# Optimization experiments

Hardware: AMD Instinct MI355X
Metric: run time of the kernel (lower is better)

Reference implementation:

```python
import jax, jax.numpy as jnp
import numpy as np

IN_DIM = 128
MEM_DIM = 256
NUM_CLASSES = 12
NUM_LEVELS = 17  # complete binary tree, N = 2**17 - 1 = 131071 nodes


def setup_inputs() -> dict:
    key = jax.random.key(0)
    ks = jax.random.split(key, 7)
    N = 2 ** NUM_LEVELS - 1
    s = 1.0 / np.sqrt(MEM_DIM)  # PyTorch LSTMCell/Linear init scale
    return {
        "x": jax.random.normal(ks[0], (N, IN_DIM), dtype=jnp.float32),
        "W_ih": jax.random.uniform(ks[1], (4 * MEM_DIM, IN_DIM), jnp.float32, -s, s),
        "b_ih": jax.random.uniform(ks[2], (4 * MEM_DIM,), jnp.float32, -s, s),
        "W_hh": jax.random.uniform(ks[3], (4 * MEM_DIM, MEM_DIM), jnp.float32, -s, s),
        "b_hh": jax.random.uniform(ks[4], (4 * MEM_DIM,), jnp.float32, -s, s),
        "W_fc": jax.random.uniform(ks[5], (NUM_CLASSES, MEM_DIM), jnp.float32, -s, s),
        "b_fc": jax.random.uniform(ks[6], (NUM_CLASSES,), jnp.float32, -s, s),
        "num_levels": NUM_LEVELS,
    }


def reference(x, W_ih, b_ih, W_hh, b_hh, W_fc, b_fc, num_levels):
    # Complete binary tree in BFS order: level l occupies nodes [2^l-1, 2^(l+1)-2];
    # children of level-l nodes are exactly the (contiguous) level-(l+1) nodes.
    mem = W_hh.shape[1]
    h_below = None
    c_below = None
    for l in reversed(range(num_levels)):
        n = 2 ** l
        x_l = x[n - 1:2 * n - 1]  # [n, in_dim] nodes at this level
        if h_below is None:  # leaves: zero child state
            ch_h = jnp.zeros((n, mem), dtype=x.dtype)
            ch_c = ch_h
        else:  # sum the two children's (h, c), as the recursion accumulates
            ch_h = h_below.reshape(n, 2, mem).sum(axis=1)
            ch_c = c_below.reshape(n, 2, mem).sum(axis=1)
        # PyTorch LSTMCell: gates = x W_ih^T + b_ih + h W_hh^T + b_hh, chunks i,f,g,o
        gates = x_l @ W_ih.T + b_ih + ch_h @ W_hh.T + b_hh  # [n, 4*mem]
        i, f, g, o = jnp.split(gates, 4, axis=-1)
        c_new = jax.nn.sigmoid(f) * ch_c + jax.nn.sigmoid(i) * jnp.tanh(g)
        h_new = jax.nn.sigmoid(o) * jnp.tanh(c_new)
        h_below, c_below = h_new, c_new
    # Original applies FC to state[1] == cell state c of the root (kept faithfully).
    return c_below[:1] @ W_fc.T + b_fc  # [1, num_classes]
```

## Files before the change

kernel.cpp:

```cpp
#include <hip/hip_runtime.h>
#include <hip/hip_bf16.h>
#include <cstddef>

#define IN_DIM 128
#define MEM 256
#define KTOT 384
#define NLEAF 65536
#define NBLK_TAIL 8

typedef float f32x4 __attribute__((ext_vector_type(4)));
typedef short s16x8 __attribute__((ext_vector_type(8)));
typedef unsigned int u32;

__device__ inline unsigned short f2bf(float f){
    unsigned int u = __builtin_bit_cast(unsigned int, f);
    u += 0x7fff + ((u >> 16) & 1);
    return (unsigned short)(u >> 16);
}

__device__ inline void gld_lds16(const void* g, void* l){
    __builtin_amdgcn_global_load_lds((const __attribute__((address_space(1))) u32*)g,
                                     (__attribute__((address_space(3))) u32*)l, 16, 0, 0);
}

__device__ inline float fsigm(float x){
    return __builtin_amdgcn_rcpf(1.f + __expf(-x));
}
__device__ inline float ftanh(float x){
    return 2.f * __builtin_amdgcn_rcpf(1.f + __expf(-2.f * x)) - 1.f;
}

__host__ __device__ inline size_t offA(int l){
    if (l == 16) return 0;
    return 8388608u + 384u * (65536u - (1u << (l + 1)));
}
#define ARENA_ELEMS 33554048u
#define ARENA_PAD   65536u

__device__ inline void grid_barrier(unsigned* ctr, unsigned target){
    __syncthreads();
    if (threadIdx.x == 0){
        __threadfence();
        __hip_atomic_fetch_add(ctr, 1u, __ATOMIC_RELEASE, __HIP_MEMORY_SCOPE_AGENT);
        while (__hip_atomic_load(ctr, __ATOMIC_RELAXED, __HIP_MEMORY_SCOPE_AGENT) < target)
            __builtin_amdgcn_s_sleep(2);
    }
    __syncthreads();
    __threadfence();
}

__global__ void pack_kernel(const float* __restrict__ x,
                            const float* __restrict__ W_ih, const float* __restrict__ b_ih,
                            const float* __restrict__ W_hh, const float* __restrict__ b_hh,
                            unsigned short* __restrict__ Wp, float* __restrict__ bp,
                            unsigned short* __restrict__ Aarena, unsigned* __restrict__ ctr){
    const int stride = gridDim.x * blockDim.x;
    const int tid0 = blockIdx.x * blockDim.x + threadIdx.x;
    if (tid0 == 0){ ctr[0] = 0; }

    for (int g = tid0; g < 1024 * 48; g += stride){
        int row = g / 48, ko = (g - row * 48) * 8;
        const float* s = (ko < IN_DIM) ? (W_ih + (size_t)row * IN_DIM + ko)
                                       : (W_hh + (size_t)row * MEM + (ko - IN_DIM));
        f32x4 v0 = *(const f32x4*)s, v1 = *(const f32x4*)(s + 4);
        s16x8 o;
        #pragma unroll
        for (int e = 0; e < 4; ++e){ o[e] = (short)f2bf(v0[e]); o[4+e] = (short)f2bf(v1[e]); }
        *(s16x8*)(Wp + (size_t)row * KTOT + ko) = o;
        if (ko == 0) bp[row] = b_ih[row] + b_hh[row];
    }

    const int TOTAL_G = 131071 * 16;
    for (int g = tid0; g < TOTAL_G; g += stride){
        int i  = g >> 4;
        int ko = (g & 15) * 8;
        int l  = 31 - __clz(i + 1);
        int j  = i + 1 - (1 << l);
        size_t dst = offA(l) + (size_t)j * ((l == 16) ? 128 : 384) + ko;
        const f32x4* s = (const f32x4*)(x + (size_t)i * IN_DIM + ko);
        f32x4 v0 = s[0], v1 = s[1];
        s16x8 o;
        #pragma unroll
        for (int e = 0; e < 4; ++e){ o[e] = (short)f2bf(v0[e]); o[4+e] = (short)f2bf(v1[e]); }
        *(s16x8*)(Aarena + dst) = o;
    }
}

#define BM 128
#define KC 64

template<int NK>
__global__ __launch_bounds__(256) void gemm_lstm_kernel(
    const unsigned short* __restrict__ A, int n,
    const unsigned short* __restrict__ Wp, const float* __restrict__ bp,
    const float* __restrict__ csum_in, int leaf,
    unsigned short* __restrict__ A_next, float* __restrict__ csum_out)
{
    __shared__ __align__(16) unsigned short As[2][BM * KC];
    __shared__ __align__(16) unsigned short Bs[2][BM * KC];

    const int tid  = threadIdx.x;
    const int lane = tid & 63;
    const int wid  = tid >> 6;
    const int wm   = wid >> 1;
    const int wc   = wid & 1;
    const int row0 = blockIdx.x * BM;
    const int m0   = blockIdx.y * 32;

    const int srow = lane >> 3;
    const int scol = ((lane & 7) ^ srow) * 8;

    const int mg = m0 + wc * 16 + (lane & 15);

    const float b0 = bp[0 * 256 + mg];
    const float b1 = bp[1 * 256 + mg];
    const float b2 = bp[2 * 256 + mg];
    const float b3 = bp[3 * 256 + mg];
    float cpre[4][4];
    if (!leaf){
        #pragma unroll
        for (int r = 0; r < 4; ++r){
            const int base = row0 + wm * 64 + r * 16 + (lane >> 4) * 4;
            #pragma unroll
            for (int e = 0; e < 4; ++e)
                cpre[r][e] = csum_in[(size_t)(base + e) * MEM + mg];
        }
    } else {
        #pragma unroll
        for (int r = 0; r < 4; ++r)
            #pragma unroll
            for (int e = 0; e < 4; ++e) cpre[r][e] = 0.f;
    }

    f32x4 acc[4][4];
    #pragma unroll
    for (int r = 0; r < 4; ++r)
        #pragma unroll
        for (int q = 0; q < 4; ++q)
            acc[r][q] = (f32x4){0.f, 0.f, 0.f, 0.f};

    auto stage = [&](int d, int kk){
        char* asb = (char*)As[d];
        char* bsb = (char*)Bs[d];
        #pragma unroll
        for (int q = 0; q < 4; ++q){
            int t = wid * 4 + q;
            int r = t * 8 + srow;
            gld_lds16(A + (size_t)(row0 + r) * NK + kk + scol, asb + t * 1024);
        }
        #pragma unroll
        for (int q = 0; q < 4; ++q){
            int t = wid * 4 + q;
            int b = t * 8 + srow;
            int grow = (b >> 5) * 256 + m0 + (b & 31);
            gld_lds16(Wp + (size_t)grow * KTOT + kk + scol, bsb + t * 1024);
        }
    };

    constexpr int nIter = NK / KC;
    stage(0, 0);
    int buf = 0;
    #pragma unroll
    for (int it = 0; it < nIter; ++it){
        if (it + 1 < nIter){
            stage(buf ^ 1, (it + 1) * KC);
            asm volatile("s_waitcnt vmcnt(8)" ::: "memory");
        } else {
            asm volatile("s_waitcnt vmcnt(0)" ::: "memory");
        }
        __builtin_amdgcn_s_barrier();
        const unsigned short* Ab = As[buf];
        const unsigned short* Bb = Bs[buf];
        #pragma unroll
        for (int ks = 0; ks < 2; ++ks){
            const int slot = ks * 4 + (lane >> 4);
            const int kb = (slot ^ (lane & 7)) * 8;
            s16x8 a[4], b[4];
            #pragma unroll
            for (int r = 0; r < 4; ++r)
                a[r] = *(const s16x8*)(Ab + (wm * 64 + r * 16 + (lane & 15)) * KC + kb);
            #pragma unroll
            for (int q = 0; q < 4; ++q)
                b[q] = *(const s16x8*)(Bb + (q * 32 + wc * 16 + (lane & 15)) * KC + kb);
            #pragma unroll
            for (int r = 0; r < 4; ++r)
                #pragma unroll
                for (int q = 0; q < 4; ++q)
                    acc[r][q] = __builtin_amdgcn_mfma_f32_16x16x32_bf16(a[r], b[q], acc[r][q], 0, 0, 0);
        }
        __builtin_amdgcn_s_barrier();
        buf ^= 1;
    }

    #pragma unroll
    for (int r = 0; r < 4; ++r){
        const int base = row0 + wm * 64 + r * 16 + (lane >> 4) * 4;
        float cn[4], hn[4];
        #pragma unroll
        for (int e = 0; e < 4; ++e){
            float iv = acc[r][0][e] + b0;
            float fv = acc[r][1][e] + b1;
            float gv = acc[r][2][e] + b2;
            float ov = acc[r][3][e] + b3;
            float c  = fsigm(fv) * cpre[r][e] + fsigm(iv) * ftanh(gv);
            cn[e] = c;
            hn[e] = fsigm(ov) * ftanh(c);
        }
        if (base < n){
            int p0 = base >> 1;
            A_next[(size_t)p0 * KTOT + IN_DIM + mg] = f2bf(hn[0] + hn[1]);
            csum_out[(size_t)p0 * MEM + mg] = cn[0] + cn[1];
        }
        if (base + 2 < n){
            int p1 = (base >> 1) + 1;
            A_next[(size_t)p1 * KTOT + IN_DIM + mg] = f2bf(hn[2] + hn[3]);
            csum_out[(size_t)p1 * MEM + mg] = cn[2] + cn[3];
        }
    }
}

__global__ __launch_bounds__(256) void tail_kernel(
    const unsigned short* __restrict__ arena,
    const unsigned short* __restrict__ Wp, const float* __restrict__ bp,
    float* cs_in, float* cs_out,
    float* __restrict__ c_root,
    const float* __restrict__ W_fc, const float* __restrict__ b_fc,
    float* __restrict__ out, unsigned* __restrict__ ctr)
{
    __shared__ __align__(16) unsigned short WpL[128 * KTOT];
    __shared__ __align__(16) unsigned short AL[64 * KTOT];

    const int tid  = threadIdx.x;
    const int lane = tid & 63;
    const int wid  = tid >> 6;
    const int wm   = wid >> 1;
    const int wc   = wid & 1;
    const int m0   = blockIdx.x * 32;
    const int mg   = m0 + wc * 16 + (lane & 15);

    #pragma unroll
    for (int i = 0; i < 24; ++i){
        int p0 = wid * 1536 + i * 64;
        int p  = p0 + lane;
        int lrow  = p / 48;
        int pslot = p % 48;
        int lslot = pslot ^ (lrow & 7);
        int grow  = (lrow >> 5) * 256 + m0 + (lrow & 31);
        gld_lds16(Wp + (size_t)grow * KTOT + lslot * 8, (char*)WpL + (size_t)p0 * 16);
    }

    const float b0 = bp[0 * 256 + mg];
    const float b1 = bp[1 * 256 + mg];
    const float b2 = bp[2 * 256 + mg];
    const float b3 = bp[3 * 256 + mg];

    asm volatile("s_waitcnt vmcnt(0)" ::: "memory");
    __builtin_amdgcn_s_barrier();

    unsigned gen = 0;
    for (int l = 7; l >= 0; --l){
        const int n = 1 << l;
        const unsigned short* Al = arena + offA(l);
        const int nhalf = (n > 64) ? (n >> 6) : 1;

        for (int h = 0; h < nhalf; ++h){
            const int r0 = h * 64;
            const int rows = (n < 64) ? n : 64;

            const int nslots = rows * 48;
            for (int t = 0; t * 256 < nslots; ++t){
                int pbase = t * 256 + wid * 64;
                int p = pbase + lane;
                if (p < nslots){
                    int row   = p / 48;
                    int pslot = p - row * 48;
                    int lslot = pslot ^ (row & 7);
                    gld_lds16(Al + (size_t)(r0 + row) * KTOT + lslot * 8,
                              (char*)AL + (size_t)pbase * 16);
                }
            }

            float cpre[2][4];
            #pragma unroll
            for (int r = 0; r < 2; ++r){
                const int base = r0 + wm * 32 + r * 16 + (lane >> 4) * 4;
                #pragma unroll
                for (int e = 0; e < 4; ++e)
                    cpre[r][e] = cs_in[(size_t)(base + e) * MEM + mg];
            }

            asm volatile("s_waitcnt vmcnt(0)" ::: "memory");
            __builtin_amdgcn_s_barrier();

            f32x4 acc[2][4];
            #pragma unroll
            for (int r = 0; r < 2; ++r)
                #pragma unroll
                for (int q = 0; q < 4; ++q)
                    acc[r][q] = (f32x4){0.f, 0.f, 0.f, 0.f};

            #pragma unroll
            for (int kc = 0; kc < 12; ++kc){
                const int ls = kc * 4 + (lane >> 4);
                const int kb = (ls ^ (lane & 7)) * 8;
                s16x8 a[2], b[4];
                #pragma unroll
                for (int r = 0; r < 2; ++r)
                    a[r] = *(const s16x8*)(AL + (size_t)(wm * 32 + r * 16 + (lane & 15)) * KTOT + kb);
                #pragma unroll
                for (int q = 0; q < 4; ++q)
                    b[q] = *(const s16x8*)(WpL + (q * 32 + wc * 16 + (lane & 15)) * KTOT + kb);
                #pragma unroll
                for (int r = 0; r < 2; ++r)
                    #pragma unroll
                    for (int q = 0; q < 4; ++q)
                        acc[r][q] = __builtin_amdgcn_mfma_f32_16x16x32_bf16(a[r], b[q], acc[r][q], 0, 0, 0);
            }

            #pragma unroll
            for (int r = 0; r < 2; ++r){
                const int base = r0 + wm * 32 + r * 16 + (lane >> 4) * 4;
                float cn[4], hn[4];
                #pragma unroll
                for (int e = 0; e < 4; ++e){
                    float iv = acc[r][0][e] + b0;
                    float fv = acc[r][1][e] + b1;
                    float gv = acc[r][2][e] + b2;
                    float ov = acc[r][3][e] + b3;
                    float c  = fsigm(fv) * cpre[r][e] + fsigm(iv) * ftanh(gv);
                    cn[e] = c;
                    hn[e] = fsigm(ov) * ftanh(c);
                }
                if (l == 0){
                    if (base == 0) c_root[mg] = cn[0];
                } else {
                    unsigned short* A_next = (unsigned short*)arena + offA(l - 1);
                    if (base < n){
                        int p0 = base >> 1;
                        A_next[(size_t)p0 * KTOT + IN_DIM + mg] = f2bf(hn[0] + hn[1]);
                        cs_out[(size_t)p0 * MEM + mg] = cn[0] + cn[1];
                    }
                    if (base + 2 < n){
                        int p1 = (base >> 1) + 1;
                        A_next[(size_t)p1 * KTOT + IN_DIM + mg] = f2bf(hn[2] + hn[3]);
                        cs_out[(size_t)p1 * MEM + mg] = cn[2] + cn[3];
                    }
                }
            }
            __builtin_amdgcn_s_barrier();
        }

        float* t = cs_in; cs_in = cs_out; cs_out = t;
        ++gen;
        grid_barrier(ctr, (unsigned)(NBLK_TAIL * gen));
    }

    if (blockIdx.x == 0){
        int w = wid;
        for (int cls = w * 3; cls < w * 3 + 3; ++cls){
            float s = 0.f;
            for (int m = lane; m < 256; m += 64)
                s += c_root[m] * W_fc[cls * 256 + m];
            #pragma unroll
            for (int off = 32; off; off >>= 1)
                s += __shfl_down(s, off, 64);
            if (lane == 0) out[cls] = s + b_fc[cls];
        }
    }
}

extern "C" void kernel_launch(void* const* d_in, const int* in_sizes, int n_in,
                              void* d_out, int out_size, void* d_ws, size_t ws_size,
                              hipStream_t stream)
{
    const float* x    = (const float*)d_in[0];
    const float* W_ih = (const float*)d_in[1];
    const float* b_ih = (const float*)d_in[2];
    const float* W_hh = (const float*)d_in[3];
    const float* b_hh = (const float*)d_in[4];
    const float* W_fc = (const float*)d_in[5];
    const float* b_fc = (const float*)d_in[6];
    float* out = (float*)d_out;

    const size_t OFF_WP = 0;
    const size_t OFF_BP = 786432;
    const size_t OFF_A  = 790528;
    const size_t OFF_CS0 = OFF_A + (size_t)(ARENA_ELEMS + ARENA_PAD) * 2;
    const size_t OFF_CS1 = OFF_CS0 + 33554432;
    const size_t OFF_CR  = OFF_CS1 + 33554432;
    const size_t OFF_CTR = OFF_CR + 1024;
    const size_t NEEDED  = OFF_CTR + 64;
    if (ws_size < NEEDED) return;

    char* ws = (char*)d_ws;
    unsigned short* Wp    = (unsigned short*)(ws + OFF_WP);
    float* bp             = (float*)(ws + OFF_BP);
    unsigned short* arena = (unsigned short*)(ws + OFF_A);
    float* cs0            = (float*)(ws + OFF_CS0);
    float* cs1            = (float*)(ws + OFF_CS1);
    float* c_root         = (float*)(ws + OFF_CR);
    unsigned* ctr         = (unsigned*)(ws + OFF_CTR);

    pack_kernel<<<dim3(2048), dim3(256), 0, stream>>>(
        x, W_ih, b_ih, W_hh, b_hh, Wp, bp, arena, ctr);

    gemm_lstm_kernel<IN_DIM><<<dim3(NLEAF / BM, 8), dim3(256), 0, stream>>>(
        arena + offA(16), NLEAF, Wp, bp,
        nullptr, 1, arena + offA(15), cs0);

    float* cs_in = cs0; float* cs_out = cs1;
    for (int l = 15; l >= 8; --l){
        int n = 1 << l;
        gemm_lstm_kernel<KTOT><<<dim3(n / BM, 8), dim3(256), 0, stream>>>(
            arena + offA(l), n, Wp, bp,
            cs_in, 0, arena + offA(l - 1), cs_out);
        float* t = cs_in; cs_in = cs_out; cs_out = t;
    }

    tail_kernel<<<dim3(NBLK_TAIL), dim3(256), 0, stream>>>(
        arena, Wp, bp, cs_in, cs_out, c_root, W_fc, b_fc, out, ctr);
}
```

Before: 220.4 us.

## Add 256x256-tile 8-wave GEMM-LSTM kernel for levels 15 and 14

Adds a new fused GEMM+LSTM kernel with 512 threads and 256-row by 64-column-per-gate tiles, using an 8-wave ping-pong schedule that stages A and B halves across barriers with swizzled LDS and setprio around the MFMA bursts. It replaces the generic 128-row kernel for the two largest non-leaf levels (15 and 14). The goal is more data reuse per LDS tile and better overlap of global-to-LDS loads with MFMA work. In exchange, the kernel needs more LDS and registers, runs one block per CU, and uses fewer blocks per level.

```diff
diff --git a/kernel.cpp b/kernel.cpp
--- a/kernel.cpp
+++ b/kernel.cpp
@@ -83,6 +83,179 @@
         #pragma unroll
         for (int e = 0; e < 4; ++e){ o[e] = (short)f2bf(v0[e]); o[4+e] = (short)f2bf(v1[e]); }
         *(s16x8*)(Aarena + dst) = o;
+    }
+}
+
+template<int NK>
+__global__ __launch_bounds__(512, 1) void gemm_lstm8p_kernel(
+    const unsigned short* __restrict__ A, int n,
+    const unsigned short* __restrict__ Wp, const float* __restrict__ bp,
+    const float* __restrict__ csum_in,
+    unsigned short* __restrict__ A_next, float* __restrict__ csum_out)
+{
+    __shared__ __align__(16) unsigned short As[2][2][128 * 64];
+    __shared__ __align__(16) unsigned short Bs[2][2][128 * 64];
+
+    const int tid  = threadIdx.x;
+    const int lane = tid & 63;
+    const int wid  = tid >> 6;
+    const int wm   = wid >> 2;
+    const int wn   = wid & 3;
+    const int row0 = blockIdx.x * 256;
+    const int m0   = blockIdx.y * 64;
+    const int mg   = m0 + wn * 16 + (lane & 15);
+
+    auto stageA = [&](int kt, int h){
+        #pragma unroll
+        for (int i = 0; i < 2; ++i){
+            int p  = i * 512 + tid;
+            int r  = p >> 3;
+            int ls = (p & 7) ^ (r & 7);
+            gld_lds16(A + (size_t)(row0 + h * 128 + r) * NK + kt * 64 + ls * 8,
+                      (char*)As[kt & 1][h] + (size_t)(i * 512 + wid * 64) * 16);
+        }
+    };
+    auto stageB = [&](int kt, int h){
+        #pragma unroll
+        for (int i = 0; i < 2; ++i){
+            int p  = i * 512 + tid;
+            int r  = p >> 3;
+            int b  = h * 128 + r;
+            int grow = (b >> 6) * 256 + m0 + (b & 63);
+            int ls = (p & 7) ^ (r & 7);
+            gld_lds16(Wp + (size_t)grow * KTOT + kt * 64 + ls * 8,
+                      (char*)Bs[kt & 1][h] + (size_t)(i * 512 + wid * 64) * 16);
+        }
+    };
+
+    f32x4 acc[8][4];
+    #pragma unroll
+    for (int r = 0; r < 8; ++r)
+        #pragma unroll
+        for (int q = 0; q < 4; ++q)
+            acc[r][q] = (f32x4){0.f, 0.f, 0.f, 0.f};
+
+    constexpr int nkt = NK / 64;
+    stageA(0, 0); stageA(0, 1); stageB(0, 0);
+    if (nkt > 1) stageB(1, 0);
+    stageB(0, 1);
+
+    s16x8 bfr[2][2];
+
+    #pragma unroll
+    for (int t = 0; t < nkt; ++t){
+        const unsigned short* Ab = As[t & 1][wm];
+        const unsigned short* Bb0 = Bs[t & 1][0];
+        const unsigned short* Bb1 = Bs[t & 1][1];
+
+        if (t + 1 < nkt) { asm volatile("s_waitcnt vmcnt(4)" ::: "memory"); }
+        else             { asm volatile("s_waitcnt vmcnt(2)" ::: "memory"); }
+        __builtin_amdgcn_s_barrier();
+        asm volatile("" ::: "memory");
+
+        #pragma unroll
+        for (int rh = 0; rh < 2; ++rh){
+            s16x8 a[4][2];
+            #pragma unroll
+            for (int j = 0; j < 4; ++j)
+                #pragma unroll
+                for (int ks = 0; ks < 2; ++ks){
+                    int kb = (((ks * 4 + (lane >> 4)) ^ (lane & 7))) * 8;
+                    a[j][ks] = *(const s16x8*)(Ab + (size_t)(rh * 64 + j * 16 + (lane & 15)) * 64 + kb);
+                }
+            if (rh == 0){
+                #pragma unroll
+                for (int q2 = 0; q2 < 2; ++q2)
+                    #pragma unroll
+                    for (int ks = 0; ks < 2; ++ks){
+                        int kb = (((ks * 4 + (lane >> 4)) ^ (lane & 7))) * 8;
+                        bfr[q2][ks] = *(const s16x8*)(Bb0 + (size_t)(q2 * 64 + wn * 16 + (lane & 15)) * 64 + kb);
+                    }
+                if (t + 1 < nkt) stageA(t + 1, 0);
+            } else {
+                if (t + 1 < nkt) stageA(t + 1, 1);
+            }
+            __builtin_amdgcn_s_setprio(1);
+            #pragma unroll
+            for (int j = 0; j < 4; ++j)
+                #pragma unroll
+                for (int q2 = 0; q2 < 2; ++q2)
+                    #pragma unroll
+                    for (int ks = 0; ks < 2; ++ks)
+                        acc[rh * 4 + j][q2] = __builtin_amdgcn_mfma_f32_16x16x32_bf16(
+                            a[j][ks], bfr[q2][ks], acc[rh * 4 + j][q2], 0, 0, 0);
+            __builtin_amdgcn_s_setprio(0);
+        }
+
+        if (t + 1 < nkt) { asm volatile("s_waitcnt vmcnt(4)" ::: "memory"); }
+        else             { asm volatile("s_waitcnt vmcnt(0)" ::: "memory"); }
+        __builtin_amdgcn_s_barrier();
+        asm volatile("" ::: "memory");
+
+        #pragma unroll
+        for (int rh = 0; rh < 2; ++rh){
+            s16x8 a[4][2];
+            #pragma unroll
+            for (int j = 0; j < 4; ++j)
+                #pragma unroll
+                for (int ks = 0; ks < 2; ++ks){
+                    int kb = (((ks * 4 + (lane >> 4)) ^ (lane & 7))) * 8;
+                    a[j][ks] = *(const s16x8*)(Ab + (size_t)(rh * 64 + j * 16 + (lane & 15)) * 64 + kb);
+                }
+            if (rh == 0){
+                #pragma unroll
+                for (int q2 = 0; q2 < 2; ++q2)
+                    #pragma unroll
+                    for (int ks = 0; ks < 2; ++ks){
+                        int kb = (((ks * 4 + (lane >> 4)) ^ (lane & 7))) * 8;
+                        bfr[q2][ks] = *(const s16x8*)(Bb1 + (size_t)(q2 * 64 + wn * 16 + (lane & 15)) * 64 + kb);
+                    }
+                if (t + 2 < nkt) stageB(t + 2, 0);
+            } else {
+                if (t + 1 < nkt) stageB(t + 1, 1);
+            }
+            __builtin_amdgcn_s_setprio(1);
+            #pragma unroll
+            for (int j = 0; j < 4; ++j)
+                #pragma unroll
+                for (int q2 = 0; q2 < 2; ++q2)
+                    #pragma unroll
+                    for (int ks = 0; ks < 2; ++ks)
+                        acc[rh * 4 + j][2 + q2] = __builtin_amdgcn_mfma_f32_16x16x32_bf16(
+                            a[j][ks], bfr[q2][ks], acc[rh * 4 + j][2 + q2], 0, 0, 0);
+            __builtin_amdgcn_s_setprio(0);
+        }
+        __builtin_amdgcn_s_barrier();
+        asm volatile("" ::: "memory");
+    }
+
+    const float b0 = bp[0 * 256 + mg];
+    const float b1 = bp[1 * 256 + mg];
+    const float b2 = bp[2 * 256 + mg];
+    const float b3 = bp[3 * 256 + mg];
+    #pragma unroll
+    for (int r = 0; r < 8; ++r){
+        const int base = row0 + wm * 128 + r * 16 + (lane >> 4) * 4;
+        float cpre[4];
+        #pragma unroll
+        for (int e = 0; e < 4; ++e)
+            cpre[e] = csum_in[(size_t)(base + e) * MEM + mg];
+        float cn[4], hn[4];
+        #pragma unroll
+        for (int e = 0; e < 4; ++e){
+            float iv = acc[r][0][e] + b0;
+            float fv = acc[r][1][e] + b1;
+            float gv = acc[r][2][e] + b2;
+            float ov = acc[r][3][e] + b3;
+            float c  = fsigm(fv) * cpre[e] + fsigm(iv) * ftanh(gv);
+            cn[e] = c;
+            hn[e] = fsigm(ov) * ftanh(c);
+        }
+        int p0 = base >> 1;
+        A_next[(size_t)p0 * KTOT + IN_DIM + mg] = f2bf(hn[0] + hn[1]);
+        csum_out[(size_t)p0 * MEM + mg] = cn[0] + cn[1];
+        A_next[(size_t)(p0 + 1) * KTOT + IN_DIM + mg] = f2bf(hn[2] + hn[3]);
+        csum_out[(size_t)(p0 + 1) * MEM + mg] = cn[2] + cn[3];
     }
 }
 
@@ -408,8 +581,13 @@
         arena + offA(16), NLEAF, Wp, bp,
         nullptr, 1, arena + offA(15), cs0);
 
+    gemm_lstm8p_kernel<KTOT><<<dim3(128, 4), dim3(512), 0, stream>>>(
+        arena + offA(15), 32768, Wp, bp, cs0, arena + offA(14), cs1);
+    gemm_lstm8p_kernel<KTOT><<<dim3(64, 4), dim3(512), 0, stream>>>(
+        arena + offA(14), 16384, Wp, bp, cs1, arena + offA(13), cs0);
+
     float* cs_in = cs0; float* cs_out = cs1;
-    for (int l = 15; l >= 8; --l){
+    for (int l = 13; l >= 8; --l){
         int n = 1 << l;
         gemm_lstm_kernel<KTOT><<<dim3(n / BM, 8), dim3(256), 0, stream>>>(
             arena + offA(l), n, Wp, bp,
```

Result: faster. 213.0 us, median of 2 (-3.4%).
